# Kernel optimization log

Hardware: AMD Instinct MI355X
Metric: run time of the kernel (lower is better)

Reference implementation:

```python
import jax, jax.numpy as jnp
import numpy as np

N, E, DIM, H = 50000, 800000, 128, 8
HD = DIM // H  # head_dim = 16
HID = 4 * DIM  # ffn hidden (hidden_dim_multiplier=4)


def setup_inputs() -> dict:
    key = jax.random.key(0)
    ks = jax.random.split(key, 12)
    s = 0.05
    return {
        "x": jax.random.normal(ks[0], (N, DIM), jnp.float32),
        "src": jax.random.randint(ks[1], (E,), 0, N, jnp.int32),
        "dst": jax.random.randint(ks[2], (E,), 0, N, jnp.int32),
        "fc_w": jax.random.normal(ks[3], (DIM, DIM), jnp.float32) * s,
        "fc_b": jax.random.normal(ks[4], (DIM,), jnp.float32) * s,
        "au_w": jax.random.normal(ks[5], (H, DIM), jnp.float32) * s,
        "au_b": jax.random.normal(ks[6], (H,), jnp.float32) * s,
        "av_w": jax.random.normal(ks[7], (H, DIM), jnp.float32) * s,
        "w1": jax.random.normal(ks[8], (HID, 4 * DIM), jnp.float32) * s,
        "b1": jax.random.normal(ks[9], (HID,), jnp.float32) * s,
        "w2": jax.random.normal(ks[10], (DIM, HID), jnp.float32) * s,
        "b2": jax.random.normal(ks[11], (DIM,), jnp.float32) * s,
    }


def reference(x, src, dst, fc_w, fc_b, au_w, au_b, av_w, w1, b1, w2, b2):
    h = x @ fc_w.T + fc_b                                   # [N, DIM]
    su = h @ au_w.T + au_b                                  # [N, H]
    sv = h @ av_w.T                                         # [N, H] (no bias)
    # u_add_v + LeakyReLU(0.2)
    scores = jax.nn.leaky_relu(su[src] + sv[dst], 0.2)      # [E, H]
    # edge_softmax grouped by destination node (stable)
    m = jax.ops.segment_max(scores, dst, num_segments=N)    # [N, H]
    ex = jnp.exp(scores - m[dst])
    den = jax.ops.segment_sum(ex, dst, num_segments=N)      # [N, H]
    probs = ex / den[dst]                                   # [E, H]
    # u_mul_e_sum over heads: x reshaped [N, head_dim, H]
    xh = h.reshape(N, HD, H)
    msg = jax.ops.segment_sum(xh[src] * probs[:, None, :], dst, num_segments=N)
    msg = msg.reshape(N, DIM)
    # copy_u_mean: mean of src features over incoming edges
    ones = jnp.ones((E,), h.dtype)
    in_deg = jax.ops.segment_sum(ones, dst, num_segments=N)   # [N]
    sum2 = jax.ops.segment_sum(xh[src], dst, num_segments=N)  # [N, HD, H]
    msg2 = (sum2 / jnp.maximum(in_deg, 1.0)[:, None, None]).reshape(N, DIM)
    # symmetric-norm message: norm = 1/sqrt(out_deg[src]*out_deg[dst])
    out_deg = jax.ops.segment_sum(ones, src, num_segments=N)  # [N]
    norm = 1.0 / jnp.sqrt(out_deg[src] * out_deg[dst])        # [E]
    msg3 = jax.ops.segment_sum(h[src] * norm[:, None], dst, num_segments=N)
    # combine + feed-forward (dropout=0 -> identity)
    cat = jnp.concatenate([h, msg, msg2, msg3], axis=1)       # [N, 4*DIM]
    f = jax.nn.gelu(cat @ w1.T + b1, approximate=False)
    return f @ w2.T + b2                                      # [N, DIM]
```

## Files before the change

kernel.cpp:

```cpp
#include <hip/hip_runtime.h>
#include <hip/hip_bf16.h>

#define NNODES 50000
#define NEDGES 800000
#define DIM 128
#define NH 8
#define HID 512
#define NB 196

typedef unsigned short ushort_t;
typedef unsigned int uint_t;
typedef __attribute__((ext_vector_type(8))) short bf16x8;
typedef __attribute__((ext_vector_type(4))) float f32x4;

__device__ __forceinline__ ushort_t f2bf_bits(float v) {
    __hip_bfloat16 b = __float2bfloat16(v);
    return *(ushort_t*)&b;
}

__global__ __launch_bounds__(256) void convert_weights_kernel(
    const float* __restrict__ fc_w, const float* __restrict__ w1,
    const float* __restrict__ w2,
    ushort_t* __restrict__ fc_wb, ushort_t* __restrict__ w1b,
    ushort_t* __restrict__ w2b)
{
    int i = blockIdx.x * 256 + threadIdx.x;
    if (i < 16384)
        ((__hip_bfloat16*)fc_wb)[i] = __float2bfloat16(fc_w[i]);
    else if (i < 278528)
        ((__hip_bfloat16*)w1b)[i - 16384] = __float2bfloat16(w1[i - 16384]);
    else if (i < 344064)
        ((__hip_bfloat16*)w2b)[i - 278528] = __float2bfloat16(w2[i - 278528]);
}

template<int AF32, int OUTF32, int ACT>
__global__ __launch_bounds__(256, 3) void gemm_mfma(
    const void* A, int lda,
    const ushort_t* __restrict__ B, int ldb,
    const float* __restrict__ bias,
    void* C, int ldc, int row0,
    int M, int K)
{
    constexpr int BM = 128, BN = 128, BK = 32, PAD = 8;
    __shared__ ushort_t As[BM][BK + PAD];
    __shared__ ushort_t Bs[BN][BK + PAD];

    const int t    = threadIdx.x;
    const int bm   = blockIdx.y * BM;
    const int bn   = blockIdx.x * BN;
    const int wid  = t >> 6, lane = t & 63;
    const int wrow = wid >> 1, wcol = wid & 1;
    const int qd   = lane >> 4, l16 = lane & 15;

    f32x4 acc[4][4];
#pragma unroll
    for (int i = 0; i < 4; ++i)
#pragma unroll
        for (int j = 0; j < 4; ++j) acc[i][j] = (f32x4){0.f, 0.f, 0.f, 0.f};

    for (int k0 = 0; k0 < K; k0 += BK) {
#pragma unroll
        for (int i = 0; i < 2; ++i) {
            int v = t + i * 256;
            int r = v >> 2, c8 = (v & 3) * 8;
            int gr = bm + r;
            if (AF32) {
                float4 f0 = make_float4(0.f, 0.f, 0.f, 0.f), f1 = f0;
                if (gr < M) {
                    const float* ap = (const float*)A + (size_t)gr * lda + k0 + c8;
                    f0 = *(const float4*)ap;
                    f1 = *(const float4*)(ap + 4);
                }
                __hip_bfloat16* dstp = (__hip_bfloat16*)&As[r][c8];
                dstp[0] = __float2bfloat16(f0.x); dstp[1] = __float2bfloat16(f0.y);
                dstp[2] = __float2bfloat16(f0.z); dstp[3] = __float2bfloat16(f0.w);
                dstp[4] = __float2bfloat16(f1.x); dstp[5] = __float2bfloat16(f1.y);
                dstp[6] = __float2bfloat16(f1.z); dstp[7] = __float2bfloat16(f1.w);
            } else {
                uint4 val = make_uint4(0u, 0u, 0u, 0u);
                if (gr < M) val = *(const uint4*)((const ushort_t*)A + (size_t)gr * lda + k0 + c8);
                *(uint4*)(&As[r][c8]) = val;
            }
        }
#pragma unroll
        for (int i = 0; i < 2; ++i) {
            int v = t + i * 256;
            int r = v >> 2, c8 = (v & 3) * 8;
            *(uint4*)(&Bs[r][c8]) = *(const uint4*)(B + (size_t)(bn + r) * ldb + k0 + c8);
        }
        __syncthreads();

        bf16x8 af[4], bfr[4];
#pragma unroll
        for (int mi = 0; mi < 4; ++mi)
            af[mi] = *(const bf16x8*)(&As[wrow * 64 + mi * 16 + l16][qd * 8]);
#pragma unroll
        for (int ni = 0; ni < 4; ++ni)
            bfr[ni] = *(const bf16x8*)(&Bs[wcol * 64 + ni * 16 + l16][qd * 8]);
#pragma unroll
        for (int mi = 0; mi < 4; ++mi)
#pragma unroll
            for (int ni = 0; ni < 4; ++ni)
                acc[mi][ni] = __builtin_amdgcn_mfma_f32_16x16x32_bf16(
                    af[mi], bfr[ni], acc[mi][ni], 0, 0, 0);
        __syncthreads();
    }

#pragma unroll
    for (int mi = 0; mi < 4; ++mi) {
#pragma unroll
        for (int r = 0; r < 4; ++r) {
            int lrow = wrow * 64 + mi * 16 + qd * 4 + r;
            int grow = bm + lrow;
            if (grow >= M) continue;
#pragma unroll
            for (int ni = 0; ni < 4; ++ni) {
                int gc = bn + wcol * 64 + ni * 16 + l16;
                float v = acc[mi][ni][r] + bias[gc];
                if (ACT == 1) v = 0.5f * v * (1.f + erff(v * 0.70710678118654752f));
                size_t off = (size_t)(row0 + grow) * ldc + gc;
                if (OUTF32) ((float*)C)[off] = v;
                else ((__hip_bfloat16*)C)[off] = __float2bfloat16(v);
            }
        }
    }
}

__global__ __launch_bounds__(512, 4) void ffn_fused_kernel(
    const ushort_t* __restrict__ cat,
    const ushort_t* __restrict__ w1b,
    const float* __restrict__ b1,
    const ushort_t* __restrict__ w2b,
    const float* __restrict__ b2,
    float* __restrict__ out, int M)
{
    constexpr int BM = 128, BK = 32, PAD = 8;
    __shared__ ushort_t As[BM][BK + PAD];
    __shared__ ushort_t Bs[128][BK + PAD];
    __shared__ ushort_t Fs[128][128 + PAD];

    const int t    = threadIdx.x;
    const int bm   = blockIdx.x * BM;
    const int wid  = t >> 6, lane = t & 63;
    const int wrow = wid >> 2;
    const int wcol = wid & 3;
    const int qd   = lane >> 4, l16 = lane & 15;

    const int sr = t >> 2, sc8 = (t & 3) * 8;

    f32x4 acc_o[4][2];
#pragma unroll
    for (int i = 0; i < 4; ++i)
#pragma unroll
        for (int j = 0; j < 2; ++j) acc_o[i][j] = (f32x4){0.f, 0.f, 0.f, 0.f};

    for (int p = 0; p < 4; ++p) {
        f32x4 acc_f[4][2];
#pragma unroll
        for (int i = 0; i < 4; ++i)
#pragma unroll
            for (int j = 0; j < 2; ++j) acc_f[i][j] = (f32x4){0.f, 0.f, 0.f, 0.f};

        for (int k0 = 0; k0 < HID; k0 += BK) {
            {
                int gr = bm + sr;
                uint4 val = make_uint4(0u, 0u, 0u, 0u);
                if (gr < M) val = *(const uint4*)(cat + (size_t)gr * HID + k0 + sc8);
                *(uint4*)(&As[sr][sc8]) = val;
                *(uint4*)(&Bs[sr][sc8]) =
                    *(const uint4*)(w1b + (size_t)(p * 128 + sr) * HID + k0 + sc8);
            }
            __syncthreads();

            bf16x8 af[4], bfr[2];
#pragma unroll
            for (int mi = 0; mi < 4; ++mi)
                af[mi] = *(const bf16x8*)(&As[wrow * 64 + mi * 16 + l16][qd * 8]);
#pragma unroll
            for (int ni = 0; ni < 2; ++ni)
                bfr[ni] = *(const bf16x8*)(&Bs[wcol * 32 + ni * 16 + l16][qd * 8]);
#pragma unroll
            for (int mi = 0; mi < 4; ++mi)
#pragma unroll
                for (int ni = 0; ni < 2; ++ni)
                    acc_f[mi][ni] = __builtin_amdgcn_mfma_f32_16x16x32_bf16(
                        af[mi], bfr[ni], acc_f[mi][ni], 0, 0, 0);
            __syncthreads();
        }

#pragma unroll
        for (int mi = 0; mi < 4; ++mi) {
#pragma unroll
            for (int r = 0; r < 4; ++r) {
                int lrow = wrow * 64 + mi * 16 + qd * 4 + r;
#pragma unroll
                for (int ni = 0; ni < 2; ++ni) {
                    int lcol = wcol * 32 + ni * 16 + l16;
                    float v = acc_f[mi][ni][r] + b1[p * 128 + lcol];
                    v = 0.5f * v * (1.f + erff(v * 0.70710678118654752f));
                    Fs[lrow][lcol] = f2bf_bits(v);
                }
            }
        }
        __syncthreads();

#pragma unroll
        for (int kk = 0; kk < 4; ++kk) {
            bf16x8 af2[4], bf2[2];
#pragma unroll
            for (int mi = 0; mi < 4; ++mi)
                af2[mi] = *(const bf16x8*)(&Fs[wrow * 64 + mi * 16 + l16][kk * 32 + qd * 8]);
#pragma unroll
            for (int ni = 0; ni < 2; ++ni) {
                int col2 = wcol * 32 + ni * 16 + l16;
                bf2[ni] = *(const bf16x8*)(w2b + (size_t)col2 * HID + p * 128 + kk * 32 + qd * 8);
            }
#pragma unroll
            for (int mi = 0; mi < 4; ++mi)
#pragma unroll
                for (int ni = 0; ni < 2; ++ni)
                    acc_o[mi][ni] = __builtin_amdgcn_mfma_f32_16x16x32_bf16(
                        af2[mi], bf2[ni], acc_o[mi][ni], 0, 0, 0);
        }
        __syncthreads();
    }

#pragma unroll
    for (int mi = 0; mi < 4; ++mi) {
#pragma unroll
        for (int r = 0; r < 4; ++r) {
            int lrow = wrow * 64 + mi * 16 + qd * 4 + r;
            int grow = bm + lrow;
            if (grow >= M) continue;
#pragma unroll
            for (int ni = 0; ni < 2; ++ni) {
                int gc = wcol * 32 + ni * 16 + l16;
                out[(size_t)grow * DIM + gc] = acc_o[mi][ni][r] + b2[gc];
            }
        }
    }
}

__global__ __launch_bounds__(256) void attn_scores_kernel(
    const ushort_t* __restrict__ hb,
    const float* __restrict__ au_w, const float* __restrict__ au_b,
    const float* __restrict__ av_w,
    float* __restrict__ su, float* __restrict__ sv, int N)
{
    const int wave = threadIdx.x >> 6;
    const int lane = threadIdx.x & 63;
    const int n = blockIdx.x * 4 + wave;
    if (n >= N) return;

    const float h0 = __bfloat162float(((const __hip_bfloat16*)hb)[(size_t)n * DIM + lane]);
    const float h1 = __bfloat162float(((const __hip_bfloat16*)hb)[(size_t)n * DIM + 64 + lane]);

    float au[NH], av[NH];
#pragma unroll
    for (int hh = 0; hh < NH; ++hh) {
        au[hh] = h0 * au_w[hh * DIM + lane] + h1 * au_w[hh * DIM + 64 + lane];
        av[hh] = h0 * av_w[hh * DIM + lane] + h1 * av_w[hh * DIM + 64 + lane];
    }
#pragma unroll
    for (int off = 32; off >= 1; off >>= 1) {
#pragma unroll
        for (int hh = 0; hh < NH; ++hh) {
            au[hh] += __shfl_down(au[hh], off, 64);
            av[hh] += __shfl_down(av[hh], off, 64);
        }
    }
    if (lane == 0) {
#pragma unroll
        for (int hh = 0; hh < NH; ++hh) {
            su[(size_t)n * NH + hh] = au[hh] + au_b[hh];
            sv[(size_t)n * NH + hh] = av[hh];
        }
    }
}

__global__ __launch_bounds__(256) void degree_count_kernel(
    const int* __restrict__ src, const int* __restrict__ dst,
    float* __restrict__ out_deg, int* __restrict__ in_cnt, int E)
{
    int e = blockIdx.x * 256 + threadIdx.x;
    if (e >= E) return;
    unsafeAtomicAdd(&out_deg[src[e]], 1.f);
    atomicAdd(&in_cnt[dst[e]], 1);
}

__global__ __launch_bounds__(256) void block_sum_kernel(
    const int* __restrict__ cnt, int* __restrict__ bsum)
{
    const int lane = threadIdx.x & 63, wid = threadIdx.x >> 6;
    int i = blockIdx.x * 256 + threadIdx.x;
    int v = (i < NNODES) ? cnt[i] : 0;
#pragma unroll
    for (int off = 32; off >= 1; off >>= 1) v += __shfl_down(v, off, 64);
    __shared__ int ws_[4];
    if (lane == 0) ws_[wid] = v;
    __syncthreads();
    if (threadIdx.x == 0) bsum[blockIdx.x] = ws_[0] + ws_[1] + ws_[2] + ws_[3];
}

__global__ __launch_bounds__(256) void block_scan_kernel(
    const int* __restrict__ bsum, int* __restrict__ boff)
{
    __shared__ int sb[256];
    const int t = threadIdx.x;
    int v = (t < NB) ? bsum[t] : 0;
    sb[t] = v;
    __syncthreads();
    for (int off = 1; off < 256; off <<= 1) {
        int u = (t >= off) ? sb[t - off] : 0;
        __syncthreads();
        sb[t] += u;
        __syncthreads();
    }
    if (t < NB) boff[t] = (t == 0) ? 0 : sb[t - 1];
}

__global__ __launch_bounds__(256) void final_scan_kernel(
    const int* __restrict__ cnt, const int* __restrict__ boff,
    int* __restrict__ rowstart)
{
    __shared__ int sb[256];
    const int t = threadIdx.x;
    const int b = blockIdx.x;
    int i = b * 256 + t;
    int v = (i < NNODES) ? cnt[i] : 0;
    sb[t] = v;
    __syncthreads();
    for (int off = 1; off < 256; off <<= 1) {
        int u = (t >= off) ? sb[t - off] : 0;
        __syncthreads();
        sb[t] += u;
        __syncthreads();
    }
    if (i < NNODES) rowstart[i] = boff[b] + sb[t] - v;
    if (b == 0 && t == 0) rowstart[NNODES] = NEDGES;
}

__global__ __launch_bounds__(256) void fill_csr_kernel(
    const int* __restrict__ src, const int* __restrict__ dst,
    const int* __restrict__ rowstart, int* __restrict__ cursor,
    int* __restrict__ esrc, int E)
{
    int e = blockIdx.x * 256 + threadIdx.x;
    if (e >= E) return;
    int d = dst[e];
    int pos = rowstart[d] + atomicAdd(&cursor[d], 1);
    esrc[pos] = src[e];
}

__device__ __forceinline__ float bf_lo(uint_t v) {
    union { uint_t i; float f; } c; c.i = v << 16; return c.f;
}
__device__ __forceinline__ float bf_hi(uint_t v) {
    union { uint_t i; float f; } c; c.i = v & 0xffff0000u; return c.f;
}
__device__ __forceinline__ void st_bf2(ushort_t* p, float a, float b) {
    __hip_bfloat16 ba = __float2bfloat16(a), bb = __float2bfloat16(b);
    uint_t v = (uint_t)(*(ushort_t*)&ba) | ((uint_t)(*(ushort_t*)&bb) << 16);
    *(uint_t*)p = v;
}

__global__ __launch_bounds__(256) void gather_aggregate_kernel(
    const int* __restrict__ rowstart, const int* __restrict__ esrc,
    const ushort_t* __restrict__ hb,
    const float* __restrict__ su, const float* __restrict__ sv,
    const float* __restrict__ out_deg,
    ushort_t* __restrict__ cat, int N)
{
    const int wave = threadIdx.x >> 6;
    const int lane = threadIdx.x & 63;
    const int n = blockIdx.x * 4 + wave;
    if (n >= N) return;

    const int d0 = lane << 1;
    const int h0 = d0 & 7;

    const int e0  = rowstart[n];
    const int deg = rowstart[n + 1] - e0;
    const float2 svv = *(const float2*)(sv + (size_t)n * NH + h0);
    const float od_d = out_deg[n];

    int es = 0;
    if (deg > 0) es = esrc[e0 + (lane < deg ? lane : deg - 1)];

    float den0 = 0.f, den1 = 0.f;
    float m0 = 0.f, m1 = 0.f, s0 = 0.f, s1 = 0.f, n0 = 0.f, n1 = 0.f;

    const int degm = deg & ~3;
    for (int j = 0; j < degm; j += 4) {
        int s4[4]; float2 su4[4]; float od4[4]; uint_t hv4[4];
#pragma unroll
        for (int u = 0; u < 4; ++u) {
            int jj = j + u;
            s4[u] = (jj < 64) ? __shfl(es, jj, 64) : esrc[e0 + jj];
        }
#pragma unroll
        for (int u = 0; u < 4; ++u) {
            su4[u] = *(const float2*)(su + (size_t)s4[u] * NH + h0);
            od4[u] = out_deg[s4[u]];
            hv4[u] = *(const uint_t*)(hb + (size_t)s4[u] * DIM + d0);
        }
#pragma unroll
        for (int u = 0; u < 4; ++u) {
            float sc0 = su4[u].x + svv.x; sc0 = sc0 < 0.f ? 0.2f * sc0 : sc0;
            float sc1 = su4[u].y + svv.y; sc1 = sc1 < 0.f ? 0.2f * sc1 : sc1;
            float ex0 = __expf(sc0), ex1 = __expf(sc1);
            den0 += ex0; den1 += ex1;
            float nrm = rsqrtf(od4[u] * od_d);
            float hs0 = bf_lo(hv4[u]), hs1 = bf_hi(hv4[u]);
            m0 += hs0 * ex0; m1 += hs1 * ex1;
            s0 += hs0;       s1 += hs1;
            n0 += hs0 * nrm; n1 += hs1 * nrm;
        }
    }
    for (int j = degm; j < deg; ++j) {
        int s = (j < 64) ? __shfl(es, j, 64) : esrc[e0 + j];
        float2 suv = *(const float2*)(su + (size_t)s * NH + h0);
        float odv  = out_deg[s];
        uint_t hv  = *(const uint_t*)(hb + (size_t)s * DIM + d0);
        float sc0 = suv.x + svv.x; sc0 = sc0 < 0.f ? 0.2f * sc0 : sc0;
        float sc1 = suv.y + svv.y; sc1 = sc1 < 0.f ? 0.2f * sc1 : sc1;
        float ex0 = __expf(sc0), ex1 = __expf(sc1);
        den0 += ex0; den1 += ex1;
        float nrm = rsqrtf(odv * od_d);
        float hs0 = bf_lo(hv), hs1 = bf_hi(hv);
        m0 += hs0 * ex0; m1 += hs1 * ex1;
        s0 += hs0;       s1 += hs1;
        n0 += hs0 * nrm; n1 += hs1 * nrm;
    }

    const float inv = 1.f / fmaxf((float)deg, 1.f);
    const float r0 = den0 > 0.f ? 1.f / den0 : 0.f;
    const float r1 = den1 > 0.f ? 1.f / den1 : 0.f;
    ushort_t* row = cat + (size_t)n * 512;
    *(uint_t*)(row + d0) = *(const uint_t*)(hb + (size_t)n * DIM + d0);
    st_bf2(row + 128 + d0, m0 * r0, m1 * r1);
    st_bf2(row + 256 + d0, s0 * inv, s1 * inv);
    st_bf2(row + 384 + d0, n0, n1);
}

extern "C" void kernel_launch(void* const* d_in, const int* in_sizes, int n_in,
                              void* d_out, int out_size, void* d_ws, size_t ws_size,
                              hipStream_t stream)
{
    const float* x    = (const float*)d_in[0];
    const int*   src  = (const int*)d_in[1];
    const int*   dst  = (const int*)d_in[2];
    const float* fc_w = (const float*)d_in[3];
    const float* fc_b = (const float*)d_in[4];
    const float* au_w = (const float*)d_in[5];
    const float* au_b = (const float*)d_in[6];
    const float* av_w = (const float*)d_in[7];
    const float* w1   = (const float*)d_in[8];
    const float* b1   = (const float*)d_in[9];
    const float* w2   = (const float*)d_in[10];
    const float* b2   = (const float*)d_in[11];
    float* out = (float*)d_out;

    const int N = NNODES, E = NEDGES;

    char* w = (char*)d_ws;
    ushort_t* fc_wb = (ushort_t*)w;  w += (size_t)DIM * DIM * 2;
    ushort_t* w1b   = (ushort_t*)w;  w += (size_t)HID * 512 * 2;
    ushort_t* w2b   = (ushort_t*)w;  w += (size_t)DIM * HID * 2;
    ushort_t* hb    = (ushort_t*)w;  w += (size_t)N * DIM * 2;
    ushort_t* cat   = (ushort_t*)w;  w += (size_t)N * 512 * 2;
    float* su       = (float*)w;     w += (size_t)N * NH * 4;
    float* sv       = (float*)w;     w += (size_t)N * NH * 4;
    float* out_deg  = (float*)w;     w += (size_t)N * 4;
    int*   in_cnt   = (int*)w;       w += (size_t)N * 4;
    int*   cursor   = (int*)w;       w += (size_t)N * 4;
    int*   rowstart = (int*)w;       w += (size_t)(N + 16) * 4;
    int*   bsum     = (int*)w;       w += (size_t)256 * 4;
    int*   boff     = (int*)w;       w += (size_t)256 * 4;
    int*   esrc     = (int*)w;       w += (size_t)E * 4;

    (void)hipMemsetAsync(out_deg, 0, (size_t)N * 3 * 4, stream);

    convert_weights_kernel<<<1344, 256, 0, stream>>>(fc_w, w1, w2, fc_wb, w1b, w2b);

    {
        dim3 g(1, (N + 127) / 128);
        gemm_mfma<1, 0, 0><<<g, 256, 0, stream>>>(x, DIM, fc_wb, DIM, fc_b,
                                                  hb, DIM, 0, N, DIM);
    }
    attn_scores_kernel<<<(N + 3) / 4, 256, 0, stream>>>(hb, au_w, au_b, av_w, su, sv, N);
    degree_count_kernel<<<(E + 255) / 256, 256, 0, stream>>>(src, dst, out_deg, in_cnt, E);
    block_sum_kernel<<<NB, 256, 0, stream>>>(in_cnt, bsum);
    block_scan_kernel<<<1, 256, 0, stream>>>(bsum, boff);
    final_scan_kernel<<<NB, 256, 0, stream>>>(in_cnt, boff, rowstart);
    fill_csr_kernel<<<(E + 255) / 256, 256, 0, stream>>>(src, dst, rowstart, cursor, esrc, E);
    gather_aggregate_kernel<<<(N + 3) / 4, 256, 0, stream>>>(
        rowstart, esrc, hb, su, sv, out_deg, cat, N);

    ffn_fused_kernel<<<(N + 127) / 128, 512, 0, stream>>>(
        cat, w1b, b1, w2b, b2, out, N);
}
```

Before: 421.7 us.

## Fuse fc GEMM with attention score projection via composed weights

Precomputes the composed matrices au_w·fc_w and av_w·fc_w, plus the matching folded biases, in a small kernel. A new fused kernel computes h and the 16 attention scores directly from x with MFMA in one pass. This removes the separate attn_scores kernel and its re-read of h. It changes the numerics slightly, because scores now come from bf16 x times the composed weights rather than from the rounded h, and the composed kernel uses a serial 128-step dot product per thread.

```diff
diff --git a/kernel.cpp b/kernel.cpp
--- a/kernel.cpp
+++ b/kernel.cpp
@@ -33,96 +33,96 @@
         ((__hip_bfloat16*)w2b)[i - 278528] = __float2bfloat16(w2[i - 278528]);
 }
 
-template<int AF32, int OUTF32, int ACT>
-__global__ __launch_bounds__(256, 3) void gemm_mfma(
-    const void* A, int lda,
-    const ushort_t* __restrict__ B, int ldb,
-    const float* __restrict__ bias,
-    void* C, int ldc, int row0,
-    int M, int K)
-{
-    constexpr int BM = 128, BN = 128, BK = 32, PAD = 8;
-    __shared__ ushort_t As[BM][BK + PAD];
-    __shared__ ushort_t Bs[BN][BK + PAD];
+__global__ __launch_bounds__(256) void compose_attn_kernel(
+    const float* __restrict__ fc_w, const float* __restrict__ fc_b,
+    const float* __restrict__ au_w, const float* __restrict__ au_b,
+    const float* __restrict__ av_w,
+    ushort_t* __restrict__ afc, float* __restrict__ abc)
+{
+    int idx = blockIdx.x * 256 + threadIdx.x;
+    if (idx < 2048) {
+        int row = idx >> 7, col = idx & 127;
+        const float* wrow = (row < 8) ? (au_w + row * DIM) : (av_w + (row - 8) * DIM);
+        float s = 0.f;
+        for (int j = 0; j < DIM; ++j) s += wrow[j] * fc_w[j * DIM + col];
+        afc[row * DIM + col] = f2bf_bits(s);
+    }
+    if (idx < 16) {
+        const float* wrow = (idx < 8) ? (au_w + idx * DIM) : (av_w + (idx - 8) * DIM);
+        float s = (idx < 8) ? au_b[idx] : 0.f;
+        for (int j = 0; j < DIM; ++j) s += wrow[j] * fc_b[j];
+        abc[idx] = s;
+    }
+}
+
+__global__ __launch_bounds__(256, 4) void fc_attn_kernel(
+    const float* __restrict__ x,
+    const ushort_t* __restrict__ fc_wb, const float* __restrict__ fc_b,
+    const ushort_t* __restrict__ afc, const float* __restrict__ abc,
+    ushort_t* __restrict__ hb, float* __restrict__ su, float* __restrict__ sv,
+    int M)
+{
+    constexpr int PAD = 8;
+    __shared__ ushort_t Ws[128][128 + PAD];
+    __shared__ ushort_t Aw[16][128 + PAD];
 
     const int t    = threadIdx.x;
-    const int bm   = blockIdx.y * BM;
-    const int bn   = blockIdx.x * BN;
     const int wid  = t >> 6, lane = t & 63;
-    const int wrow = wid >> 1, wcol = wid & 1;
     const int qd   = lane >> 4, l16 = lane & 15;
 
-    f32x4 acc[4][4];
-#pragma unroll
-    for (int i = 0; i < 4; ++i)
-#pragma unroll
-        for (int j = 0; j < 4; ++j) acc[i][j] = (f32x4){0.f, 0.f, 0.f, 0.f};
-
-    for (int k0 = 0; k0 < K; k0 += BK) {
-#pragma unroll
-        for (int i = 0; i < 2; ++i) {
-            int v = t + i * 256;
-            int r = v >> 2, c8 = (v & 3) * 8;
-            int gr = bm + r;
-            if (AF32) {
-                float4 f0 = make_float4(0.f, 0.f, 0.f, 0.f), f1 = f0;
-                if (gr < M) {
-                    const float* ap = (const float*)A + (size_t)gr * lda + k0 + c8;
-                    f0 = *(const float4*)ap;
-                    f1 = *(const float4*)(ap + 4);
-                }
-                __hip_bfloat16* dstp = (__hip_bfloat16*)&As[r][c8];
-                dstp[0] = __float2bfloat16(f0.x); dstp[1] = __float2bfloat16(f0.y);
-                dstp[2] = __float2bfloat16(f0.z); dstp[3] = __float2bfloat16(f0.w);
-                dstp[4] = __float2bfloat16(f1.x); dstp[5] = __float2bfloat16(f1.y);
-                dstp[6] = __float2bfloat16(f1.z); dstp[7] = __float2bfloat16(f1.w);
-            } else {
-                uint4 val = make_uint4(0u, 0u, 0u, 0u);
-                if (gr < M) val = *(const uint4*)((const ushort_t*)A + (size_t)gr * lda + k0 + c8);
-                *(uint4*)(&As[r][c8]) = val;
-            }
-        }
-#pragma unroll
-        for (int i = 0; i < 2; ++i) {
-            int v = t + i * 256;
-            int r = v >> 2, c8 = (v & 3) * 8;
-            *(uint4*)(&Bs[r][c8]) = *(const uint4*)(B + (size_t)(bn + r) * ldb + k0 + c8);
-        }
-        __syncthreads();
-
-        bf16x8 af[4], bfr[4];
-#pragma unroll
-        for (int mi = 0; mi < 4; ++mi)
-            af[mi] = *(const bf16x8*)(&As[wrow * 64 + mi * 16 + l16][qd * 8]);
-#pragma unroll
-        for (int ni = 0; ni < 4; ++ni)
-            bfr[ni] = *(const bf16x8*)(&Bs[wcol * 64 + ni * 16 + l16][qd * 8]);
-#pragma unroll
-        for (int mi = 0; mi < 4; ++mi)
-#pragma unroll
-            for (int ni = 0; ni < 4; ++ni)
-                acc[mi][ni] = __builtin_amdgcn_mfma_f32_16x16x32_bf16(
-                    af[mi], bfr[ni], acc[mi][ni], 0, 0, 0);
-        __syncthreads();
-    }
-
-#pragma unroll
-    for (int mi = 0; mi < 4; ++mi) {
-#pragma unroll
-        for (int r = 0; r < 4; ++r) {
-            int lrow = wrow * 64 + mi * 16 + qd * 4 + r;
-            int grow = bm + lrow;
-            if (grow >= M) continue;
-#pragma unroll
-            for (int ni = 0; ni < 4; ++ni) {
-                int gc = bn + wcol * 64 + ni * 16 + l16;
-                float v = acc[mi][ni][r] + bias[gc];
-                if (ACT == 1) v = 0.5f * v * (1.f + erff(v * 0.70710678118654752f));
-                size_t off = (size_t)(row0 + grow) * ldc + gc;
-                if (OUTF32) ((float*)C)[off] = v;
-                else ((__hip_bfloat16*)C)[off] = __float2bfloat16(v);
-            }
-        }
+#pragma unroll
+    for (int i = 0; i < 8; ++i) {
+        int v = t + i * 256;
+        int row = v >> 4, ch = v & 15;
+        *(uint4*)(&Ws[row][ch * 8]) = *(const uint4*)(fc_wb + row * 128 + ch * 8);
+    }
+    {
+        int row = t >> 4, ch = t & 15;
+        *(uint4*)(&Aw[row][ch * 8]) = *(const uint4*)(afc + row * 128 + ch * 8);
+    }
+    __syncthreads();
+
+    const int tile = blockIdx.x * 4 + wid;
+    if (tile * 16 >= M) return;
+
+    const int arow = tile * 16 + l16;
+    const float* xp = x + (size_t)arow * DIM + qd * 8;
+    const float cb = abc[l16];
+
+    f32x4 acc[8], accs;
+#pragma unroll
+    for (int i = 0; i < 8; ++i) acc[i] = (f32x4){0.f, 0.f, 0.f, 0.f};
+    accs = (f32x4){0.f, 0.f, 0.f, 0.f};
+
+#pragma unroll
+    for (int ks = 0; ks < 4; ++ks) {
+        float4 f0 = *(const float4*)(xp + ks * 32);
+        float4 f1 = *(const float4*)(xp + ks * 32 + 4);
+        union { ushort_t u[8]; bf16x8 v; } a;
+        a.u[0] = f2bf_bits(f0.x); a.u[1] = f2bf_bits(f0.y);
+        a.u[2] = f2bf_bits(f0.z); a.u[3] = f2bf_bits(f0.w);
+        a.u[4] = f2bf_bits(f1.x); a.u[5] = f2bf_bits(f1.y);
+        a.u[6] = f2bf_bits(f1.z); a.u[7] = f2bf_bits(f1.w);
+#pragma unroll
+        for (int nf = 0; nf < 8; ++nf) {
+            bf16x8 bw = *(const bf16x8*)(&Ws[nf * 16 + l16][ks * 32 + qd * 8]);
+            acc[nf] = __builtin_amdgcn_mfma_f32_16x16x32_bf16(a.v, bw, acc[nf], 0, 0, 0);
+        }
+        bf16x8 ba = *(const bf16x8*)(&Aw[l16][ks * 32 + qd * 8]);
+        accs = __builtin_amdgcn_mfma_f32_16x16x32_bf16(a.v, ba, accs, 0, 0, 0);
+    }
+
+#pragma unroll
+    for (int r = 0; r < 4; ++r) {
+        int grow = tile * 16 + qd * 4 + r;
+#pragma unroll
+        for (int nf = 0; nf < 8; ++nf) {
+            int gc = nf * 16 + l16;
+            hb[(size_t)grow * DIM + gc] = f2bf_bits(acc[nf][r] + fc_b[gc]);
+        }
+        float vs = accs[r] + cb;
+        if (l16 < 8) su[(size_t)grow * NH + l16] = vs;
+        else         sv[(size_t)grow * NH + (l16 - 8)] = vs;
     }
 }
 
@@ -237,43 +237,6 @@
                 int gc = wcol * 32 + ni * 16 + l16;
                 out[(size_t)grow * DIM + gc] = acc_o[mi][ni][r] + b2[gc];
             }
-        }
-    }
-}
-
-__global__ __launch_bounds__(256) void attn_scores_kernel(
-    const ushort_t* __restrict__ hb,
-    const float* __restrict__ au_w, const float* __restrict__ au_b,
-    const float* __restrict__ av_w,
-    float* __restrict__ su, float* __restrict__ sv, int N)
-{
-    const int wave = threadIdx.x >> 6;
-    const int lane = threadIdx.x & 63;
-    const int n = blockIdx.x * 4 + wave;
-    if (n >= N) return;
-
-    const float h0 = __bfloat162float(((const __hip_bfloat16*)hb)[(size_t)n * DIM + lane]);
-    const float h1 = __bfloat162float(((const __hip_bfloat16*)hb)[(size_t)n * DIM + 64 + lane]);
-
-    float au[NH], av[NH];
-#pragma unroll
-    for (int hh = 0; hh < NH; ++hh) {
-        au[hh] = h0 * au_w[hh * DIM + lane] + h1 * au_w[hh * DIM + 64 + lane];
-        av[hh] = h0 * av_w[hh * DIM + lane] + h1 * av_w[hh * DIM + 64 + lane];
-    }
-#pragma unroll
-    for (int off = 32; off >= 1; off >>= 1) {
-#pragma unroll
-        for (int hh = 0; hh < NH; ++hh) {
-            au[hh] += __shfl_down(au[hh], off, 64);
-            av[hh] += __shfl_down(av[hh], off, 64);
-        }
-    }
-    if (lane == 0) {
-#pragma unroll
-        for (int hh = 0; hh < NH; ++hh) {
-            su[(size_t)n * NH + hh] = au[hh] + au_b[hh];
-            sv[(size_t)n * NH + hh] = av[hh];
         }
     }
 }
@@ -467,6 +430,8 @@
     ushort_t* fc_wb = (ushort_t*)w;  w += (size_t)DIM * DIM * 2;
     ushort_t* w1b   = (ushort_t*)w;  w += (size_t)HID * 512 * 2;
     ushort_t* w2b   = (ushort_t*)w;  w += (size_t)DIM * HID * 2;
+    ushort_t* afc   = (ushort_t*)w;  w += (size_t)16 * DIM * 2;
+    float* abc      = (float*)w;     w += (size_t)16 * 4;
     ushort_t* hb    = (ushort_t*)w;  w += (size_t)N * DIM * 2;
     ushort_t* cat   = (ushort_t*)w;  w += (size_t)N * 512 * 2;
     float* su       = (float*)w;     w += (size_t)N * NH * 4;
@@ -482,13 +447,11 @@
     (void)hipMemsetAsync(out_deg, 0, (size_t)N * 3 * 4, stream);
 
     convert_weights_kernel<<<1344, 256, 0, stream>>>(fc_w, w1, w2, fc_wb, w1b, w2b);
-
-    {
-        dim3 g(1, (N + 127) / 128);
-        gemm_mfma<1, 0, 0><<<g, 256, 0, stream>>>(x, DIM, fc_wb, DIM, fc_b,
-                                                  hb, DIM, 0, N, DIM);
-    }
-    attn_scores_kernel<<<(N + 3) / 4, 256, 0, stream>>>(hb, au_w, au_b, av_w, su, sv, N);
+    compose_attn_kernel<<<8, 256, 0, stream>>>(fc_w, fc_b, au_w, au_b, av_w, afc, abc);
+
+    fc_attn_kernel<<<(N / 16 + 3) / 4, 256, 0, stream>>>(
+        x, fc_wb, fc_b, afc, abc, hb, su, sv, N);
+
     degree_count_kernel<<<(E + 255) / 256, 256, 0, stream>>>(src, dst, out_deg, in_cnt, E);
     block_sum_kernel<<<NB, 256, 0, stream>>>(in_cnt, bsum);
     block_scan_kernel<<<1, 256, 0, stream>>>(bsum, boff);
```

New measurement: 374.2 us. 1.13x faster.
